# Kernel tuning notes

Hardware: AMD Instinct MI355X
Metric: run time of the kernel (lower is better)

## Reference

```python
import jax, jax.numpy as jnp
import numpy as np

N_NODES = 100000
N_EDGES = 1600000
N_FEAT = 128
HIDDEN = 64


def gcn_conv(x, W, b, src, dst, ew, n_nodes):
    """Faithful PyG GCNConv with edge_weight and default add_self_loops=True.

    out[i] = sum_{(j->i) in E} norm_ji * (x_j @ W^T) + d_i^{-1} * (x_i @ W^T) + b
    where deg_i = 1 + sum of incoming edge weights (self-loop weight 1),
    norm_ji = deg_j^{-1/2} * ew_ji * deg_i^{-1/2}.
    """
    xw = x @ W.T  # [N, H] -- transform first (PyG applies lin before propagate)
    deg = jnp.ones((n_nodes,), x.dtype) + jax.ops.segment_sum(ew, dst, num_segments=n_nodes)
    dis = jnp.where(deg > 0, jax.lax.rsqrt(deg), 0.0)  # deg^{-1/2}
    norm = dis[src] * ew * dis[dst]  # [E]
    msgs = norm[:, None] * xw[src]  # [E, H] gathered messages
    agg = jax.ops.segment_sum(msgs, dst, num_segments=n_nodes)  # scatter-add at targets
    agg = agg + (dis * dis)[:, None] * xw  # self-loop contribution (weight 1)
    return agg + b


def setup_inputs() -> dict:
    key = jax.random.key(0)
    k1, k2, k3, k4, k5, k6, k7, k8 = jax.random.split(key, 8)
    x = jax.random.normal(k1, (N_NODES, N_FEAT), dtype=jnp.float32)
    edge_index = jax.random.randint(k2, (2, N_EDGES), 0, N_NODES, dtype=jnp.int64)
    edge_attr = jax.random.uniform(k3, (N_EDGES,), dtype=jnp.float32)
    batch = jnp.zeros((N_NODES,), dtype=jnp.int64)
    s1 = 1.0 / np.sqrt(N_FEAT)
    s2 = 1.0 / np.sqrt(HIDDEN)
    W1 = jax.random.uniform(k4, (HIDDEN, N_FEAT), jnp.float32, -s1, s1)
    b1 = jnp.zeros((HIDDEN,), jnp.float32)
    W2 = jax.random.uniform(k5, (HIDDEN, HIDDEN), jnp.float32, -s2, s2)
    b2 = jnp.zeros((HIDDEN,), jnp.float32)
    W3 = jax.random.uniform(k6, (1, HIDDEN), jnp.float32, -s2, s2)
    b3 = jax.random.uniform(k7, (1,), jnp.float32, -s2, s2)
    return {"x": x, "edge_index": edge_index, "edge_attr": edge_attr, "batch": batch,
            "W1": W1, "b1": b1, "W2": W2, "b2": b2, "W3": W3, "b3": b3}


def reference(x, edge_index, edge_attr, batch, W1, b1, W2, b2, W3, b3):
    src, dst = edge_index[0], edge_index[1]
    n = x.shape[0]
    h = jax.nn.relu(gcn_conv(x, W1, b1, src, dst, edge_attr, n))
    h = jax.nn.relu(gcn_conv(h, W2, b2, src, dst, edge_attr, n))
    return h @ W3.T + b3  # [N, 1]
```

## Files before the change

### kernel.cpp

```cpp
#include <hip/hip_runtime.h>
#include <hip/hip_fp16.h>

#define NFEAT 128
#define HID 64
#define CAP 64


__device__ __forceinline__ float4 ld_h4(const uint2* __restrict__ p, size_t idx) {
    uint2 u = p[idx];
    __half2 a = *reinterpret_cast<const __half2*>(&u.x);
    __half2 b = *reinterpret_cast<const __half2*>(&u.y);
    float2 fa = __half22float2(a);
    float2 fb = __half22float2(b);
    return make_float4(fa.x, fa.y, fb.x, fb.y);
}


template <int K, bool HALF_OUT>
__device__ __forceinline__ void xw_body(const float* __restrict__ x,
                                        const float* __restrict__ W,
                                        void* __restrict__ outv, int M,
                                        int bidx, int tid) {
    int lane = tid & 63;
    int cg = __builtin_amdgcn_readfirstlane(tid >> 6);
    int row = bidx * 64 + lane;
    if (row >= M) return;

    const float4* xr = (const float4*)(x + (size_t)row * K);
    const float4* Wr = (const float4*)(W + (size_t)cg * 16 * K);

    float acc[16];
#pragma unroll
    for (int h = 0; h < 16; ++h) acc[h] = 0.0f;

#pragma unroll 4
    for (int kc = 0; kc < K / 4; ++kc) {
        float4 xv = xr[kc];
#pragma unroll
        for (int h = 0; h < 16; ++h) {
            float4 wv = Wr[h * (K / 4) + kc];
            acc[h] = fmaf(xv.x, wv.x, acc[h]);
            acc[h] = fmaf(xv.y, wv.y, acc[h]);
            acc[h] = fmaf(xv.z, wv.z, acc[h]);
            acc[h] = fmaf(xv.w, wv.w, acc[h]);
        }
    }

    if (HALF_OUT) {
        __half2 hp[8];
#pragma unroll
        for (int j = 0; j < 8; ++j)
            hp[j] = __float22half2_rn(make_float2(acc[2 * j], acc[2 * j + 1]));
        uint4 u0 = make_uint4(*(unsigned*)&hp[0], *(unsigned*)&hp[1],
                              *(unsigned*)&hp[2], *(unsigned*)&hp[3]);
        uint4 u1 = make_uint4(*(unsigned*)&hp[4], *(unsigned*)&hp[5],
                              *(unsigned*)&hp[6], *(unsigned*)&hp[7]);
        uint4* o = (uint4*)((char*)outv + (size_t)row * 128 + cg * 32);
        o[0] = u0;
        o[1] = u1;
    } else {
        float* out = (float*)outv;
        float4* o = (float4*)(out + (size_t)row * HID + cg * 16);
#pragma unroll
        for (int q = 0; q < 4; ++q)
            o[q] = make_float4(acc[4 * q], acc[4 * q + 1], acc[4 * q + 2], acc[4 * q + 3]);
    }
}


__global__ __launch_bounds__(256) void k_fill_xw(const int* __restrict__ src,
                                                 const int* __restrict__ dst,
                                                 const float* __restrict__ ew,
                                                 int* cnt, unsigned* __restrict__ csr,
                                                 const float* __restrict__ x,
                                                 const float* __restrict__ W1,
                                                 void* __restrict__ xwout,
                                                 int ne, int gFill, int M) {
    if ((int)blockIdx.x < gFill) {
        int e = blockIdx.x * 256 + threadIdx.x;
        if (e < ne) {
            int d = dst[e];
            unsigned q = __float2uint_rn(ew[e] * 32767.0f);
            int slot = atomicAdd(&cnt[d], 1);
            if (slot < CAP)
                csr[((size_t)d << 6) + slot] = ((unsigned)src[e] & 0x1FFFFu) | (q << 17);
        }
    } else {
        xw_body<NFEAT, true>(x, W1, xwout, M, blockIdx.x - gFill, threadIdx.x);
    }
}


__global__ __launch_bounds__(256) void k_deg(const int* __restrict__ cnt,
                                             const unsigned* __restrict__ csr,
                                             float* __restrict__ dis, int n) {
    int i = blockIdx.x * 256 + threadIdx.x;
    if (i >= n) return;
    int c = min(cnt[i], CAP);
    const uint4* row = (const uint4*)(csr + ((size_t)i << 6));
    float s = 0.0f;
    int rounds = (c + 3) >> 2;
    for (int r = 0; r < rounds; ++r) {
        uint4 u = row[r];
        int b = r * 4;
        s += (b + 0 < c) ? (float)(u.x >> 17) : 0.0f;
        s += (b + 1 < c) ? (float)(u.y >> 17) : 0.0f;
        s += (b + 2 < c) ? (float)(u.z >> 17) : 0.0f;
        s += (b + 3 < c) ? (float)(u.w >> 17) : 0.0f;
    }
    dis[i] = rsqrtf(1.0f + s * (1.0f / 32767.0f));
}


__global__ __launch_bounds__(256) void k_xw2(const uint2* __restrict__ xh,
                                             const float* __restrict__ W,
                                             uint2* __restrict__ out, int M) {
    int lane = threadIdx.x & 63;
    int cg = __builtin_amdgcn_readfirstlane(threadIdx.x >> 6);
    int row = blockIdx.x * 64 + lane;
    if (row >= M) return;

    const uint2* xr = xh + (size_t)row * 16;
    const float4* Wr = (const float4*)(W + (size_t)cg * 16 * HID);

    float acc[16];
#pragma unroll
    for (int h = 0; h < 16; ++h) acc[h] = 0.0f;

#pragma unroll 4
    for (int kc = 0; kc < 16; ++kc) {
        float4 xv = ld_h4(xr, kc);
#pragma unroll
        for (int h = 0; h < 16; ++h) {
            float4 wv = Wr[h * 16 + kc];
            acc[h] = fmaf(xv.x, wv.x, acc[h]);
            acc[h] = fmaf(xv.y, wv.y, acc[h]);
            acc[h] = fmaf(xv.z, wv.z, acc[h]);
            acc[h] = fmaf(xv.w, wv.w, acc[h]);
        }
    }

    __half2 hp[8];
#pragma unroll
    for (int j = 0; j < 8; ++j)
        hp[j] = __float22half2_rn(make_float2(acc[2 * j], acc[2 * j + 1]));
    uint4 u0 = make_uint4(*(unsigned*)&hp[0], *(unsigned*)&hp[1],
                          *(unsigned*)&hp[2], *(unsigned*)&hp[3]);
    uint4 u1 = make_uint4(*(unsigned*)&hp[4], *(unsigned*)&hp[5],
                          *(unsigned*)&hp[6], *(unsigned*)&hp[7]);
    uint4* o = (uint4*)((char*)out + (size_t)row * 128 + cg * 32);
    o[0] = u0;
    o[1] = u1;
}


__device__ __forceinline__ float4 gather_node_h(const uint2* __restrict__ xwh,
                                                const float* __restrict__ dis,
                                                const int* __restrict__ cnt,
                                                const unsigned* __restrict__ csr,
                                                int i, int fq) {
    float di = dis[i];
    float4 sv = ld_h4(xwh, (size_t)i * 16 + fq);
    float s = di * di;
    float4 acc = make_float4(s * sv.x, s * sv.y, s * sv.z, s * sv.w);

    int c = min(cnt[i], CAP);
    const uint4* row = (const uint4*)(csr + ((size_t)i << 6));
    int rounds = (c + 3) >> 2;
    const float inv = 1.0f / 32767.0f;
    for (int r = 0; r < rounds; ++r) {
        uint4 u = row[r];
        int b = r * 4;
        unsigned s0 = u.x & 0x1FFFFu, s1 = u.y & 0x1FFFFu;
        unsigned s2 = u.z & 0x1FFFFu, s3 = u.w & 0x1FFFFu;
        float n0 = (b + 0 < c) ? dis[s0] * ((float)(u.x >> 17) * inv) * di : 0.0f;
        float n1 = (b + 1 < c) ? dis[s1] * ((float)(u.y >> 17) * inv) * di : 0.0f;
        float n2 = (b + 2 < c) ? dis[s2] * ((float)(u.z >> 17) * inv) * di : 0.0f;
        float n3 = (b + 3 < c) ? dis[s3] * ((float)(u.w >> 17) * inv) * di : 0.0f;
        float4 v0 = ld_h4(xwh, (size_t)s0 * 16 + fq);
        float4 v1 = ld_h4(xwh, (size_t)s1 * 16 + fq);
        float4 v2 = ld_h4(xwh, (size_t)s2 * 16 + fq);
        float4 v3 = ld_h4(xwh, (size_t)s3 * 16 + fq);
        acc.x = fmaf(n0, v0.x, acc.x);
        acc.y = fmaf(n0, v0.y, acc.y);
        acc.z = fmaf(n0, v0.z, acc.z);
        acc.w = fmaf(n0, v0.w, acc.w);
        acc.x = fmaf(n1, v1.x, acc.x);
        acc.y = fmaf(n1, v1.y, acc.y);
        acc.z = fmaf(n1, v1.z, acc.z);
        acc.w = fmaf(n1, v1.w, acc.w);
        acc.x = fmaf(n2, v2.x, acc.x);
        acc.y = fmaf(n2, v2.y, acc.y);
        acc.z = fmaf(n2, v2.z, acc.z);
        acc.w = fmaf(n2, v2.w, acc.w);
        acc.x = fmaf(n3, v3.x, acc.x);
        acc.y = fmaf(n3, v3.y, acc.y);
        acc.z = fmaf(n3, v3.z, acc.z);
        acc.w = fmaf(n3, v3.w, acc.w);
    }
    return acc;
}


__global__ __launch_bounds__(256) void k_gather1(const uint2* __restrict__ xwh,
                                                 const float* __restrict__ dis,
                                                 const int* __restrict__ cnt,
                                                 const unsigned* __restrict__ csr,
                                                 const float* __restrict__ b1,
                                                 uint2* __restrict__ out, int n) {
    int lane = threadIdx.x & 63;
    int g    = lane >> 4;
    int fq   = lane & 15;
    int wid   = (blockIdx.x * 256 + threadIdx.x) >> 6;
    int nwave = (gridDim.x * 256) >> 6;
    float4 bq = ((const float4*)b1)[fq];

    for (int i0 = wid * 4; i0 < n; i0 += nwave * 4) {
        int i = i0 + g;
        if (i >= n) continue;
        float4 acc = gather_node_h(xwh, dis, cnt, csr, i, fq);
        __half2 lo = __float22half2_rn(make_float2(fmaxf(acc.x + bq.x, 0.0f),
                                                   fmaxf(acc.y + bq.y, 0.0f)));
        __half2 hi = __float22half2_rn(make_float2(fmaxf(acc.z + bq.z, 0.0f),
                                                   fmaxf(acc.w + bq.w, 0.0f)));
        out[(size_t)i * 16 + fq] = make_uint2(*(unsigned*)&lo, *(unsigned*)&hi);
    }
}


__global__ __launch_bounds__(256) void k_gather2(const uint2* __restrict__ xwh,
                                                 const float* __restrict__ dis,
                                                 const int* __restrict__ cnt,
                                                 const unsigned* __restrict__ csr,
                                                 const float* __restrict__ b2,
                                                 const float* __restrict__ W3,
                                                 const float* __restrict__ b3,
                                                 float* __restrict__ out, int n) {
    int lane = threadIdx.x & 63;
    int g    = lane >> 4;
    int fq   = lane & 15;
    int wid   = (blockIdx.x * 256 + threadIdx.x) >> 6;
    int nwave = (gridDim.x * 256) >> 6;
    float4 bq = ((const float4*)b2)[fq];
    float4 wq = ((const float4*)W3)[fq];
    float bb3 = b3[0];

    for (int i0 = wid * 4; i0 < n; i0 += nwave * 4) {
        int i = i0 + g;
        if (i >= n) continue;
        float4 acc = gather_node_h(xwh, dis, cnt, csr, i, fq);
        float p = fmaxf(acc.x + bq.x, 0.0f) * wq.x
                + fmaxf(acc.y + bq.y, 0.0f) * wq.y
                + fmaxf(acc.z + bq.z, 0.0f) * wq.z
                + fmaxf(acc.w + bq.w, 0.0f) * wq.w;
        p += __shfl_xor(p, 1, 64);
        p += __shfl_xor(p, 2, 64);
        p += __shfl_xor(p, 4, 64);
        p += __shfl_xor(p, 8, 64);
        if (fq == 0) out[i] = p + bb3;
    }
}


__global__ __launch_bounds__(256) void k_xw_f32(const float* __restrict__ x,
                                                const float* __restrict__ W,
                                                float* __restrict__ out, int M, int K_is_128) {
    if (K_is_128)
        xw_body<NFEAT, false>(x, W, out, M, blockIdx.x, threadIdx.x);
    else
        xw_body<HID, false>(x, W, out, M, blockIdx.x, threadIdx.x);
}

__global__ __launch_bounds__(256) void k_deg_init1(float* deg, int n) {
    int i = blockIdx.x * 256 + threadIdx.x;
    if (i < n) deg[i] = 1.0f;
}

__global__ __launch_bounds__(256) void k_deg_accum(const int* __restrict__ dst,
                                                   const float* __restrict__ ew,
                                                   float* deg, int ne) {
    int e = blockIdx.x * 256 + threadIdx.x;
    if (e < ne) atomicAdd(&deg[dst[e]], ew[e]);
}

__global__ __launch_bounds__(256) void k_rsqrt(float* deg, int n) {
    int i = blockIdx.x * 256 + threadIdx.x;
    if (i < n) deg[i] = rsqrtf(deg[i]);
}

__global__ __launch_bounds__(256) void k_selfinit(const float* __restrict__ xw,
                                                  const float* __restrict__ dis,
                                                  float* __restrict__ agg, int n) {
    int idx = blockIdx.x * 256 + threadIdx.x;
    if (idx < n * 16) {
        int i = idx >> 4;
        float d = dis[i];
        float s = d * d;
        float4 v = ((const float4*)xw)[idx];
        ((float4*)agg)[idx] = make_float4(s * v.x, s * v.y, s * v.z, s * v.w);
    }
}

__global__ __launch_bounds__(256) void k_scatter(const int* __restrict__ src,
                                                 const int* __restrict__ dst,
                                                 const float* __restrict__ ew,
                                                 const float* __restrict__ dis,
                                                 const float* __restrict__ xw,
                                                 float* __restrict__ agg, int ne) {
    int t = threadIdx.x;
    int e = blockIdx.x * 4 + (t >> 6);
    if (e >= ne) return;
    int s = src[e], d = dst[e];
    float nrm = dis[s] * ew[e] * dis[d];
    int h = t & 63;
    atomicAdd(&agg[(size_t)d * HID + h], nrm * xw[(size_t)s * HID + h]);
}

__global__ __launch_bounds__(256) void k_bias_relu(float* __restrict__ agg,
                                                   const float* __restrict__ b, int n) {
    int idx = blockIdx.x * 256 + threadIdx.x;
    if (idx < n * 16) {
        int hq = idx & 15;
        float4 v = ((float4*)agg)[idx];
        float4 bb = ((const float4*)b)[hq];
        v.x = fmaxf(v.x + bb.x, 0.0f);
        v.y = fmaxf(v.y + bb.y, 0.0f);
        v.z = fmaxf(v.z + bb.z, 0.0f);
        v.w = fmaxf(v.w + bb.w, 0.0f);
        ((float4*)agg)[idx] = v;
    }
}

__global__ __launch_bounds__(256) void k_final(const float* __restrict__ agg,
                                               const float* __restrict__ b2,
                                               const float* __restrict__ W3,
                                               const float* __restrict__ b3,
                                               float* __restrict__ out, int n) {
    int t = threadIdx.x;
    int i = blockIdx.x * 4 + (t >> 6);
    if (i >= n) return;
    int h = t & 63;
    float v = fmaxf(agg[(size_t)i * HID + h] + b2[h], 0.0f) * W3[h];
#pragma unroll
    for (int off = 32; off > 0; off >>= 1) v += __shfl_down(v, off, 64);
    if (h == 0) out[i] = v + b3[0];
}


extern "C" void kernel_launch(void* const* d_in, const int* in_sizes, int n_in,
                              void* d_out, int out_size, void* d_ws, size_t ws_size,
                              hipStream_t stream) {
    const float* x  = (const float*)d_in[0];
    const int*   ei = (const int*)d_in[1];
    const float* ew = (const float*)d_in[2];
    const float* W1 = (const float*)d_in[4];
    const float* b1 = (const float*)d_in[5];
    const float* W2 = (const float*)d_in[6];
    const float* b2 = (const float*)d_in[7];
    const float* W3 = (const float*)d_in[8];
    const float* b3 = (const float*)d_in[9];
    float* out = (float*)d_out;

    int N = in_sizes[0] / NFEAT;
    int E = in_sizes[1] / 2;
    const int* src = ei;
    const int* dst = ei + E;

    dim3 blk(256);
    int gN    = (N + 255) / 256;
    int gE    = (E + 255) / 256;
    int gXW   = (N + 63) / 64;

    size_t offA   = 0;
    size_t offB   = offA + (size_t)N * HID * 2;
    size_t offDis = offB + (size_t)N * HID * 2;
    size_t offCnt = offDis + (size_t)N * 4;
    size_t offCSR = offCnt + (size_t)N * 4;
    size_t need   = offCSR + (size_t)N * CAP * 4;

    char* ws = (char*)d_ws;

    if (ws_size >= need) {
        void*     bufA = (void*)(ws + offA);
        uint2*    bufB = (uint2*)(ws + offB);
        float*    dis  = (float*)(ws + offDis);
        int*      cnt  = (int*)(ws + offCnt);
        unsigned* csr  = (unsigned*)(ws + offCSR);

        hipMemsetAsync(cnt, 0, (size_t)N * 4, stream);
        k_fill_xw<<<gE + gXW, blk, 0, stream>>>(src, dst, ew, cnt, csr,
                                                x, W1, bufA, E, gE, N);
        k_deg<<<gN, blk, 0, stream>>>(cnt, csr, dis, N);
        k_gather1<<<2048, blk, 0, stream>>>((const uint2*)bufA, dis, cnt, csr,
                                            b1, bufB, N);
        k_xw2<<<gXW, blk, 0, stream>>>((const uint2*)bufB, W2, (uint2*)bufA, N);
        k_gather2<<<2048, blk, 0, stream>>>((const uint2*)bufA, dis, cnt, csr,
                                            b2, W3, b3, out, N);
    } else {
        size_t foffA   = 0;
        size_t foffB   = foffA + (size_t)N * HID * 4;
        size_t foffDis = foffB + (size_t)N * HID * 4;
        float* bufA = (float*)(ws + foffA);
        float* bufB = (float*)(ws + foffB);
        float* dis  = (float*)(ws + foffDis);

        int gNH4 = (N * 16 + 255) / 256;
        int gE4  = (E + 3) / 4;
        int gN4  = (N + 3) / 4;
        k_deg_init1<<<gN, blk, 0, stream>>>(dis, N);
        k_deg_accum<<<gE, blk, 0, stream>>>(dst, ew, dis, E);
        k_rsqrt<<<gN, blk, 0, stream>>>(dis, N);

        k_xw_f32<<<gXW, blk, 0, stream>>>(x, W1, bufA, N, 1);
        k_selfinit<<<gNH4, blk, 0, stream>>>(bufA, dis, bufB, N);
        k_scatter<<<gE4, blk, 0, stream>>>(src, dst, ew, dis, bufA, bufB, E);
        k_bias_relu<<<gNH4, blk, 0, stream>>>(bufB, b1, N);

        k_xw_f32<<<gXW, blk, 0, stream>>>(bufB, W2, bufA, N, 0);
        k_selfinit<<<gNH4, blk, 0, stream>>>(bufA, dis, bufB, N);
        k_scatter<<<gE4, blk, 0, stream>>>(src, dst, ew, dis, bufA, bufB, E);
        k_final<<<gN4, blk, 0, stream>>>(bufB, b2, W3, b3, out, N);
    }
}
```

Baseline: 318.5 us.

## Split fused fill/xw kernel and stage x rows in LDS for layer-1 transform

Splits the combined CSR-fill and layer-1 X·W1 kernel into two separate launches. The new k_xw1 loads a 64-row tile of x into padded shared memory with coalesced loads, then each lane reads its row from LDS instead of doing strided per-row global loads. This targets uncoalesced global reads in the transform, at the cost of an extra launch and losing the overlap between the atomic-heavy fill and the compute-bound transform.

```diff
diff --git a/kernel.cpp b/kernel.cpp
--- a/kernel.cpp
+++ b/kernel.cpp
@@ -16,29 +16,57 @@
 }
 
 
-template <int K, bool HALF_OUT>
-__device__ __forceinline__ void xw_body(const float* __restrict__ x,
-                                        const float* __restrict__ W,
-                                        void* __restrict__ outv, int M,
-                                        int bidx, int tid) {
+__global__ __launch_bounds__(256) void k_fill(const int* __restrict__ src,
+                                              const int* __restrict__ dst,
+                                              const float* __restrict__ ew,
+                                              int* cnt, unsigned* __restrict__ csr,
+                                              int ne) {
+    int e = blockIdx.x * 256 + threadIdx.x;
+    if (e < ne) {
+        int d = dst[e];
+        unsigned q = __float2uint_rn(ew[e] * 32767.0f);
+        int slot = atomicAdd(&cnt[d], 1);
+        if (slot < CAP)
+            csr[((size_t)d << 6) + slot] = ((unsigned)src[e] & 0x1FFFFu) | (q << 17);
+    }
+}
+
+
+__global__ __launch_bounds__(256) void k_xw1(const float* __restrict__ x,
+                                             const float* __restrict__ W,
+                                             void* __restrict__ outv, int M) {
+    __shared__ float4 xt[64 * 33];
+    int tid = threadIdx.x;
+    int base = blockIdx.x * 64;
+
+    const float4* x4 = (const float4*)x;
+#pragma unroll
+    for (int j = 0; j < 8; ++j) {
+        int idx = j * 256 + tid;
+        int r = idx >> 5, c = idx & 31;
+        float4 v = make_float4(0.f, 0.f, 0.f, 0.f);
+        if (base + r < M) v = x4[(size_t)(base + r) * 32 + c];
+        xt[r * 33 + c] = v;
+    }
+    __syncthreads();
+
     int lane = tid & 63;
     int cg = __builtin_amdgcn_readfirstlane(tid >> 6);
-    int row = bidx * 64 + lane;
+    int row = base + lane;
     if (row >= M) return;
 
-    const float4* xr = (const float4*)(x + (size_t)row * K);
-    const float4* Wr = (const float4*)(W + (size_t)cg * 16 * K);
+    const float4* Wr = (const float4*)(W + (size_t)cg * 16 * NFEAT);
 
     float acc[16];
 #pragma unroll
     for (int h = 0; h < 16; ++h) acc[h] = 0.0f;
 
 #pragma unroll 4
-    for (int kc = 0; kc < K / 4; ++kc) {
-        float4 xv = xr[kc];
+    for (int kc = 0; kc < 32; ++kc) {
+        float4 xv = xt[lane * 33 + kc];
 #pragma unroll
         for (int h = 0; h < 16; ++h) {
-            float4 wv = Wr[h * (K / 4) + kc];
+            float4 wv = Wr[h * 32 + kc];
             acc[h] = fmaf(xv.x, wv.x, acc[h]);
             acc[h] = fmaf(xv.y, wv.y, acc[h]);
             acc[h] = fmaf(xv.z, wv.z, acc[h]);
@@ -46,48 +74,17 @@
         }
     }
 
-    if (HALF_OUT) {
-        __half2 hp[8];
-#pragma unroll
-        for (int j = 0; j < 8; ++j)
-            hp[j] = __float22half2_rn(make_float2(acc[2 * j], acc[2 * j + 1]));
-        uint4 u0 = make_uint4(*(unsigned*)&hp[0], *(unsigned*)&hp[1],
-                              *(unsigned*)&hp[2], *(unsigned*)&hp[3]);
-        uint4 u1 = make_uint4(*(unsigned*)&hp[4], *(unsigned*)&hp[5],
-                              *(unsigned*)&hp[6], *(unsigned*)&hp[7]);
-        uint4* o = (uint4*)((char*)outv + (size_t)row * 128 + cg * 32);
-        o[0] = u0;
-        o[1] = u1;
-    } else {
-        float* out = (float*)outv;
-        float4* o = (float4*)(out + (size_t)row * HID + cg * 16);
-#pragma unroll
-        for (int q = 0; q < 4; ++q)
-            o[q] = make_float4(acc[4 * q], acc[4 * q + 1], acc[4 * q + 2], acc[4 * q + 3]);
-    }
-}
-
-
-__global__ __launch_bounds__(256) void k_fill_xw(const int* __restrict__ src,
-                                                 const int* __restrict__ dst,
-                                                 const float* __restrict__ ew,
-                                                 int* cnt, unsigned* __restrict__ csr,
-                                                 const float* __restrict__ x,
-                                                 const float* __restrict__ W1,
-                                                 void* __restrict__ xwout,
-                                                 int ne, int gFill, int M) {
-    if ((int)blockIdx.x < gFill) {
-        int e = blockIdx.x * 256 + threadIdx.x;
-        if (e < ne) {
-            int d = dst[e];
-            unsigned q = __float2uint_rn(ew[e] * 32767.0f);
-            int slot = atomicAdd(&cnt[d], 1);
-            if (slot < CAP)
-                csr[((size_t)d << 6) + slot] = ((unsigned)src[e] & 0x1FFFFu) | (q << 17);
-        }
-    } else {
-        xw_body<NFEAT, true>(x, W1, xwout, M, blockIdx.x - gFill, threadIdx.x);
-    }
+    __half2 hp[8];
+#pragma unroll
+    for (int j = 0; j < 8; ++j)
+        hp[j] = __float22half2_rn(make_float2(acc[2 * j], acc[2 * j + 1]));
+    uint4 u0 = make_uint4(*(unsigned*)&hp[0], *(unsigned*)&hp[1],
+                          *(unsigned*)&hp[2], *(unsigned*)&hp[3]);
+    uint4 u1 = make_uint4(*(unsigned*)&hp[4], *(unsigned*)&hp[5],
+                          *(unsigned*)&hp[6], *(unsigned*)&hp[7]);
+    uint4* o = (uint4*)((char*)outv + (size_t)row * 128 + cg * 32);
+    o[0] = u0;
+    o[1] = u1;
 }
 
 
@@ -262,13 +259,45 @@
 }
 
 
+template <int K>
+__device__ __forceinline__ void xw_body_f32(const float* __restrict__ x,
+                                            const float* __restrict__ W,
+                                            float* __restrict__ out, int M,
+                                            int bidx, int tid) {
+    int lane = tid & 63;
+    int cg = __builtin_amdgcn_readfirstlane(tid >> 6);
+    int row = bidx * 64 + lane;
+    if (row >= M) return;
+    const float4* xr = (const float4*)(x + (size_t)row * K);
+    const float4* Wr = (const float4*)(W + (size_t)cg * 16 * K);
+    float acc[16];
+#pragma unroll
+    for (int h = 0; h < 16; ++h) acc[h] = 0.0f;
+#pragma unroll 4
+    for (int kc = 0; kc < K / 4; ++kc) {
+        float4 xv = xr[kc];
+#pragma unroll
+        for (int h = 0; h < 16; ++h) {
+            float4 wv = Wr[h * (K / 4) + kc];
+            acc[h] = fmaf(xv.x, wv.x, acc[h]);
+            acc[h] = fmaf(xv.y, wv.y, acc[h]);
+            acc[h] = fmaf(xv.z, wv.z, acc[h]);
+            acc[h] = fmaf(xv.w, wv.w, acc[h]);
+        }
+    }
+    float4* o = (float4*)(out + (size_t)row * HID + cg * 16);
+#pragma unroll
+    for (int q = 0; q < 4; ++q)
+        o[q] = make_float4(acc[4 * q], acc[4 * q + 1], acc[4 * q + 2], acc[4 * q + 3]);
+}
+
 __global__ __launch_bounds__(256) void k_xw_f32(const float* __restrict__ x,
                                                 const float* __restrict__ W,
                                                 float* __restrict__ out, int M, int K_is_128) {
     if (K_is_128)
-        xw_body<NFEAT, false>(x, W, out, M, blockIdx.x, threadIdx.x);
+        xw_body_f32<NFEAT>(x, W, out, M, blockIdx.x, threadIdx.x);
     else
-        xw_body<HID, false>(x, W, out, M, blockIdx.x, threadIdx.x);
+        xw_body_f32<HID>(x, W, out, M, blockIdx.x, threadIdx.x);
 }
 
 __global__ __launch_bounds__(256) void k_deg_init1(float* deg, int n) {
@@ -367,9 +396,9 @@
     const int* dst = ei + E;
 
     dim3 blk(256);
-    int gN    = (N + 255) / 256;
-    int gE    = (E + 255) / 256;
-    int gXW   = (N + 63) / 64;
+    int gN  = (N + 255) / 256;
+    int gE  = (E + 255) / 256;
+    int gXW = (N + 63) / 64;
 
     size_t offA   = 0;
     size_t offB   = offA + (size_t)N * HID * 2;
@@ -388,8 +417,8 @@
         unsigned* csr  = (unsigned*)(ws + offCSR);
 
         hipMemsetAsync(cnt, 0, (size_t)N * 4, stream);
-        k_fill_xw<<<gE + gXW, blk, 0, stream>>>(src, dst, ew, cnt, csr,
-                                                x, W1, bufA, E, gE, N);
+        k_fill<<<gE, blk, 0, stream>>>(src, dst, ew, cnt, csr, E);
+        k_xw1<<<gXW, blk, 0, stream>>>(x, W1, bufA, N);
         k_deg<<<gN, blk, 0, stream>>>(cnt, csr, dis, N);
         k_gather1<<<2048, blk, 0, stream>>>((const uint2*)bufA, dis, cnt, csr,
                                             b1, bufB, N);
```

New measurement: 326.5 us. 2.5% more time.
